# Kernel optimization log

Measured on AMD Instinct MI355X. Metric: run time of the kernel, lower is better.

Reference implementation:

```python
import jax, jax.numpy as jnp
import numpy as np
from math import factorial, sqrt, pi

L = 10  # must match init_kwargs


def setup_inputs() -> dict:
    key = jax.random.key(0)
    pos = jax.random.normal(key, (2_000_000, 3), dtype=jnp.float32)
    return {"pos": pos}


def _cpow_tables(zr, zi, nmax):
    """Powers (zr + i*zi)^n for n=0..nmax. Returns (nmax+1, N) real and imag parts.
    Matches powcmplx in the source (repeated complex multiply), computed once."""
    reals = [jnp.ones_like(zr)]
    imags = [jnp.zeros_like(zr)]
    for _ in range(nmax):
        r, im = reals[-1], imags[-1]
        reals.append(zr * r - zi * im)
        imags.append(zr * im + zi * r)
    return jnp.stack(reals), jnp.stack(imags)


def reference(pos):
    norms = jnp.linalg.norm(pos, axis=1)            # (N,)
    mask = (norms > 0).astype(pos.dtype)            # replaces boolean indexing ids
    x, y, x0 = pos[:, 0], pos[:, 1], pos[:, 2]
    xpl1r, xpl1i = -0.5 * x, -0.5 * y
    xm1r, xm1i = 0.5 * x, -0.5 * y
    # precompute all needed complex powers (same math as powcmplx, deduplicated)
    z1r_t, z1i_t = _cpow_tables(xpl1r, xpl1i, L)    # (L+1, N)
    z2r_t, z2i_t = _cpow_tables(xm1r, xm1i, L)

    clms = [None] * ((L + 1) ** 2)
    i = 0
    for l in range(L + 1):
        rl = norms ** l
        for M in range(-l, 1):
            m = abs(M)
            shr = jnp.zeros_like(x)
            shi = jnp.zeros_like(x)
            for p in range(l + 1):
                q = p - m
                s = l - p - q
                if q >= 0 and s >= 0:
                    z1r, z1i = z1r_t[p], z1i_t[p]
                    z2r, z2i = z2r_t[q], z2i_t[q]
                    # NOTE: faithful to source, including its quirks:
                    # zreal uses z1r**2 - z2i**2, and the term is scaled by x0
                    # (x0**s is computed in the source but never used).
                    zreal = z1r ** 2 - z2i ** 2
                    zimag = z1r * z2i + z1i * z2r
                    c = 1.0 / (factorial(p) * factorial(q) * factorial(s))
                    shr = shr + zreal * x0 * c
                    shi = shi + zimag * x0 * c
            scale = sqrt(factorial(l + m) * factorial(l - m)) * sqrt((2 * l + 1) / (4.0 * pi))
            clm_r = jnp.sum(shr * rl * mask) * scale
            clm_i = jnp.sum(shi * rl * mask) * scale
            if m == 0:
                clms[i] = clm_r
            else:
                f = sqrt(2.0) * (-1) ** m
                clms[i] = f * clm_i
                clms[i + 2 * m] = f * clm_r
            i += 1
        i += l
    return jnp.stack(clms).reshape(-1, 1)  # ((L+1)^2, 1)
```

## Files before the change

### kernel.cpp

```cpp
#include <hip/hip_runtime.h>

namespace {

constexpr int LMAX  = 10;
constexpr int NPART = 2;
constexpr int PART_OF_L[LMAX + 1] = {1, 1, 0, 0, 1, 1, 0, 0, 1, 1, 0};
constexpr double PI_D = 3.14159265358979323846;

constexpr double dfact(int n) {
    double r = 1.0;
    for (int i = 2; i <= n; ++i) r *= (double)i;
    return r;
}

constexpr double csqrt(double x) {
    if (x <= 0.0) return 0.0;
    double g = x > 1.0 ? x : 1.0;
    for (int i = 0; i < 100; ++i) g = 0.5 * (g + x / g);
    return g;
}

constexpr double FACT[LMAX + 1] = {1., 1., 2., 6., 24., 120., 720., 5040., 40320., 362880., 3628800.};

constexpr int slot_base(int part, int l) {
    int c = 0;
    for (int ll = 0; ll < l; ++ll)
        if (PART_OF_L[ll] == part) c += 2 * ll + 1;
    return c;
}
constexpr int nacc_part(int part) {
    int c = 0;
    for (int l = 0; l <= LMAX; ++l)
        if (PART_OF_L[l] == part) c += 2 * l + 1;
    return c;
}
constexpr int part_lmax(int part) {
    int mx = 0;
    for (int l = 0; l <= LMAX; ++l)
        if (PART_OF_L[l] == part) mx = l;
    return mx;
}
constexpr int slot_r(int part, int l, int m) { return slot_base(part, l) + m; }
constexpr int slot_i(int part, int l, int m) { return slot_base(part, l) + (l + 1) + (m - 1); }

constexpr int MAXNA = 61;

constexpr float ci_coef(int l, int m, int q) {
    const double c = 1.0 / (FACT[q + m] * FACT[q] * FACT[l - m - 2 * q]);
    return (q & 1) ? (float)(-c) : (float)c;
}

struct Tables {
    int   map[NPART][MAXNA];
    float scl[NPART][MAXNA];
};

constexpr Tables make_tables() {
    Tables t{};
    for (int part = 0; part < NPART; ++part) {
        for (int l = 0; l <= LMAX; ++l) {
            if (PART_OF_L[l] != part) continue;
            for (int m = 0; m <= l; ++m) {
                const int k = slot_r(part, l, m);
                const double scale =
                    csqrt(dfact(l + m) * dfact(l - m)) * csqrt((2 * l + 1) / (4.0 * PI_D));
                const double fold = (m >= 1 && (l - m) <= 1) ? 1.0 / (dfact(m) * dfact(l - m)) : 1.0;
                if (m == 0) {
                    t.map[part][k] = l * l + l;
                    t.scl[part][k] = (float)(scale * fold);
                } else {
                    const double f = csqrt(2.0) * ((m & 1) ? -1.0 : 1.0);
                    t.map[part][k] = l * l + l + m;
                    t.scl[part][k] = (float)(f * scale * fold);
                }
            }
            for (int m = 1; m <= l; ++m) {
                const int k = slot_i(part, l, m);
                const double scale =
                    csqrt(dfact(l + m) * dfact(l - m)) * csqrt((2 * l + 1) / (4.0 * PI_D));
                const double f    = csqrt(2.0) * ((m & 1) ? -1.0 : 1.0);
                const double fold = ((l - m) <= 1) ? 1.0 / (dfact(m) * dfact(l - m)) : 1.0;
                t.map[part][k] = l * l + l - m;
                t.scl[part][k] = (float)(f * scale * fold);
            }
        }
    }
    return t;
}

__constant__ Tables c_tab = make_tables();

}

template <int PART>
__device__ __forceinline__ void sht_part(const float* __restrict__ pos,
                                         float* __restrict__ out, int n, int nblk) {
    constexpr int NA = nacc_part(PART);
    constexpr int PL = part_lmax(PART);

    float acc[NA];
#pragma unroll
    for (int k = 0; k < NA; ++k) acc[k] = 0.f;

    const int bid    = (int)(blockIdx.x >> 1);
    const int tid    = bid * 256 + (int)threadIdx.x;
    const int stride = nblk * 256;

    int   i = tid;
    float x = 0.f, y = 0.f, z0 = 0.f;
    if (i < n) {
        x  = pos[3 * i + 0];
        y  = pos[3 * i + 1];
        z0 = pos[3 * i + 2];
    }

    while (i < n) {
        const int inext = i + stride;
        float     px = 0.f, py = 0.f, pz = 0.f;
        if (inext < n) {
            px = pos[3 * inext + 0];
            py = pos[3 * inext + 1];
            pz = pos[3 * inext + 2];
        }

        const float r2  = x * x + y * y + z0 * z0;
        const float nrm = sqrtf(r2);
        const float w0  = (nrm > 0.f) ? z0 : 0.f;

        const float ar = -0.5f * x, ai = -0.5f * y;
        const float rho = ar * ar + ai * ai;

        float zi[PL + 1], sr[PL + 1], si[PL + 1];
        zi[0] = 0.f;
        sr[0] = 1.f;
        si[0] = 0.f;
        float zrc = 1.f;
#pragma unroll
        for (int p = 1; p <= PL; ++p) {
            const float nzr = ar * zrc - ai * zi[p - 1];
            zi[p]           = ar * zi[p - 1] + ai * zrc;
            zrc             = nzr;
            sr[p]           = zrc * zrc;
            si[p]           = zi[p] * zi[p];
        }
        float rp[PL + 1];
        rp[0] = 1.f;
#pragma unroll
        for (int l = 1; l <= PL; ++l) rp[l] = rp[l - 1] * nrm;

#pragma unroll
        for (int l = 0; l <= LMAX; ++l) {
            if (PART_OF_L[l] != PART) continue;
            const float wrl = w0 * rp[l];
#pragma unroll
            for (int m = 0; m <= l; ++m) {
                const int Q = (l - m) >> 1;
                if (m >= 1 && Q == 0) {
                    acc[slot_r(PART, l, m)] += sr[m] * wrl;
                    acc[slot_i(PART, l, m)] += zi[m] * wrl;
                } else {
                    float shr = 0.f;
#pragma unroll
                    for (int p = m; 2 * p <= l + m; ++p) {
                        const int   q  = p - m;
                        const float cr = (float)(1.0 / (FACT[p] * FACT[q] * FACT[l - 2 * p + m]));
                        shr += (sr[p] - si[q]) * cr;
                    }
                    acc[slot_r(PART, l, m)] += shr * wrl;
                    if (m >= 1) {
                        float t = ci_coef(l, m, Q);
#pragma unroll
                        for (int q = Q - 1; q >= 0; --q) t = t * rho + ci_coef(l, m, q);
                        acc[slot_i(PART, l, m)] += (t * zi[m]) * wrl;
                    }
                }
            }
        }

        i  = inext;
        x  = px;
        y  = py;
        z0 = pz;
    }

    __shared__ float red[4][NA];
    const int lane = threadIdx.x & 63;
    const int wav  = threadIdx.x >> 6;
#pragma unroll
    for (int k = 0; k < NA; ++k) {
        float v = acc[k];
#pragma unroll
        for (int off = 32; off > 0; off >>= 1) v += __shfl_down(v, off, 64);
        if (lane == 0) red[wav][k] = v;
    }
    __syncthreads();
    if ((int)threadIdx.x < NA) {
        const int   k = (int)threadIdx.x;
        const float v = red[0][k] + red[1][k] + red[2][k] + red[3][k];
        atomicAdd(&out[c_tab.map[PART][k]], v * c_tab.scl[PART][k]);
    }
}

__global__ __launch_bounds__(256, 3) void sht_kernel(const float* __restrict__ pos,
                                                     float* __restrict__ out, int n, int nblk) {
    if (blockIdx.x & 1)
        sht_part<1>(pos, out, n, nblk);
    else
        sht_part<0>(pos, out, n, nblk);
}

extern "C" void kernel_launch(void* const* d_in, const int* in_sizes, int n_in,
                              void* d_out, int out_size, void* d_ws, size_t ws_size,
                              hipStream_t stream) {
    const float* pos = (const float*)d_in[0];
    float* out       = (float*)d_out;
    const int n      = in_sizes[0] / 3;

    hipMemsetAsync(d_out, 0, (size_t)out_size * sizeof(float), stream);

    const int threads       = 256;
    const int nblk_per_part = 384;
    const int blocks        = NPART * nblk_per_part;
    sht_kernel<<<blocks, threads, 0, stream>>>(pos, out, n, nblk_per_part);
}
```

Measured before the change: 123.5 us.

## Process two particles per thread iteration with vectorized float2 loads

Each thread now handles a pair of particles per loop iteration, loading six floats as three float2 values and interleaving the two particles' arithmetic to expose instruction-level parallelism. The si table is shrunk to only the needed entries, and only the radial powers that are actually used are computed. Launch bounds drop from 3 to 2 blocks per CU to make room for the extra registers. The aim is to hide latency through ILP and cut load instructions, at the cost of higher register pressure and lower occupancy, with the same grid size leaving half the threads idle per pair count.

```diff
diff --git a/kernel.cpp b/kernel.cpp
--- a/kernel.cpp
+++ b/kernel.cpp
@@ -39,6 +39,18 @@
     for (int l = 0; l <= LMAX; ++l)
         if (PART_OF_L[l] == part) mx = l;
     return mx;
+}
+constexpr int nls(int part) {
+    int c = 0;
+    for (int l = 0; l <= LMAX; ++l)
+        if (PART_OF_L[l] == part) ++c;
+    return c;
+}
+constexpr int lidx(int part, int l) {
+    int c = 0;
+    for (int ll = 0; ll < l; ++ll)
+        if (PART_OF_L[ll] == part) ++c;
+    return c;
 }
 constexpr int slot_r(int part, int l, int m) { return slot_base(part, l) + m; }
 constexpr int slot_i(int part, int l, int m) { return slot_base(part, l) + (l + 1) + (m - 1); }
@@ -90,6 +102,22 @@
 
 __constant__ Tables c_tab = make_tables();
 
+__device__ __forceinline__ void load_pair(const float* __restrict__ pos, int ip, int n,
+                                          float* __restrict__ c) {
+    const int i0 = 2 * ip;
+    if (i0 + 1 < n) {
+        const float2* p2 = reinterpret_cast<const float2*>(pos + 3 * i0);
+        const float2  a = p2[0], b = p2[1], d = p2[2];
+        c[0] = a.x; c[1] = a.y; c[2] = b.x;
+        c[3] = b.y; c[4] = d.x; c[5] = d.y;
+    } else if (i0 < n) {
+        c[0] = pos[3 * i0]; c[1] = pos[3 * i0 + 1]; c[2] = pos[3 * i0 + 2];
+        c[3] = c[4] = c[5] = 0.f;
+    } else {
+        c[0] = c[1] = c[2] = c[3] = c[4] = c[5] = 0.f;
+    }
+}
+
 }
 
 template <int PART>
@@ -97,6 +125,8 @@
                                          float* __restrict__ out, int n, int nblk) {
     constexpr int NA = nacc_part(PART);
     constexpr int PL = part_lmax(PART);
+    constexpr int QX = PL / 2;
+    constexpr int NL = nls(PART);
 
     float acc[NA];
 #pragma unroll
@@ -105,82 +135,121 @@
     const int bid    = (int)(blockIdx.x >> 1);
     const int tid    = bid * 256 + (int)threadIdx.x;
     const int stride = nblk * 256;
-
-    int   i = tid;
-    float x = 0.f, y = 0.f, z0 = 0.f;
-    if (i < n) {
-        x  = pos[3 * i + 0];
-        y  = pos[3 * i + 1];
-        z0 = pos[3 * i + 2];
-    }
-
-    while (i < n) {
-        const int inext = i + stride;
-        float     px = 0.f, py = 0.f, pz = 0.f;
-        if (inext < n) {
-            px = pos[3 * inext + 0];
-            py = pos[3 * inext + 1];
-            pz = pos[3 * inext + 2];
-        }
-
-        const float r2  = x * x + y * y + z0 * z0;
-        const float nrm = sqrtf(r2);
-        const float w0  = (nrm > 0.f) ? z0 : 0.f;
-
-        const float ar = -0.5f * x, ai = -0.5f * y;
-        const float rho = ar * ar + ai * ai;
-
-        float zi[PL + 1], sr[PL + 1], si[PL + 1];
-        zi[0] = 0.f;
-        sr[0] = 1.f;
-        si[0] = 0.f;
-        float zrc = 1.f;
+    const int npair  = (n + 1) >> 1;
+
+    float cur[6];
+    int   ip = tid;
+    load_pair(pos, ip, n, cur);
+
+    while (ip < npair) {
+        const int inext = ip + stride;
+        float     nxt[6];
+        load_pair(pos, inext, n, nxt);
+
+        const float X[2] = {cur[0], cur[3]};
+        const float Y[2] = {cur[1], cur[4]};
+        const float Z[2] = {cur[2], cur[5]};
+
+        float nrm[2], w0[2], ar[2], ai[2], rho[2];
+#pragma unroll
+        for (int j = 0; j < 2; ++j) {
+            const float r2 = X[j] * X[j] + Y[j] * Y[j] + Z[j] * Z[j];
+            nrm[j] = sqrtf(r2);
+            w0[j]  = (nrm[j] > 0.f) ? Z[j] : 0.f;
+            ar[j]  = -0.5f * X[j];
+            ai[j]  = -0.5f * Y[j];
+            rho[j] = ar[j] * ar[j] + ai[j] * ai[j];
+        }
+
+        float zi[2][PL + 1], sr[2][PL + 1], si[2][QX + 1], zrc[2];
+#pragma unroll
+        for (int j = 0; j < 2; ++j) {
+            zi[j][0] = 0.f;
+            sr[j][0] = 1.f;
+            si[j][0] = 0.f;
+            zrc[j]   = 1.f;
+        }
 #pragma unroll
         for (int p = 1; p <= PL; ++p) {
-            const float nzr = ar * zrc - ai * zi[p - 1];
-            zi[p]           = ar * zi[p - 1] + ai * zrc;
-            zrc             = nzr;
-            sr[p]           = zrc * zrc;
-            si[p]           = zi[p] * zi[p];
-        }
-        float rp[PL + 1];
-        rp[0] = 1.f;
-#pragma unroll
-        for (int l = 1; l <= PL; ++l) rp[l] = rp[l - 1] * nrm;
+#pragma unroll
+            for (int j = 0; j < 2; ++j) {
+                const float nzr = ar[j] * zrc[j] - ai[j] * zi[j][p - 1];
+                zi[j][p]        = ar[j] * zi[j][p - 1] + ai[j] * zrc[j];
+                zrc[j]          = nzr;
+                sr[j][p]        = zrc[j] * zrc[j];
+                if (p <= QX) si[j][p] = zi[j][p] * zi[j][p];
+            }
+        }
+
+        float wl[2][NL];
+#pragma unroll
+        for (int j = 0; j < 2; ++j) {
+            if constexpr (PART == 0) {
+                const float n1 = nrm[j], n2 = n1 * n1, n3 = n2 * n1;
+                const float n6 = n3 * n3, n7 = n6 * n1, n10 = n7 * n3;
+                wl[j][0] = w0[j] * n2;
+                wl[j][1] = w0[j] * n3;
+                wl[j][2] = w0[j] * n6;
+                wl[j][3] = w0[j] * n7;
+                wl[j][4] = w0[j] * n10;
+            } else {
+                const float n1 = nrm[j], n2 = n1 * n1, n4 = n2 * n2;
+                const float n5 = n4 * n1, n8 = n4 * n4, n9 = n8 * n1;
+                wl[j][0] = w0[j];
+                wl[j][1] = w0[j] * n1;
+                wl[j][2] = w0[j] * n4;
+                wl[j][3] = w0[j] * n5;
+                wl[j][4] = w0[j] * n8;
+                wl[j][5] = w0[j] * n9;
+            }
+        }
 
 #pragma unroll
         for (int l = 0; l <= LMAX; ++l) {
             if (PART_OF_L[l] != PART) continue;
-            const float wrl = w0 * rp[l];
+            const int li = lidx(PART, l);
 #pragma unroll
             for (int m = 0; m <= l; ++m) {
                 const int Q = (l - m) >> 1;
                 if (m >= 1 && Q == 0) {
-                    acc[slot_r(PART, l, m)] += sr[m] * wrl;
-                    acc[slot_i(PART, l, m)] += zi[m] * wrl;
+#pragma unroll
+                    for (int j = 0; j < 2; ++j)
+                        acc[slot_r(PART, l, m)] += sr[j][m] * wl[j][li];
+#pragma unroll
+                    for (int j = 0; j < 2; ++j)
+                        acc[slot_i(PART, l, m)] += zi[j][m] * wl[j][li];
                 } else {
-                    float shr = 0.f;
+                    float shr[2] = {0.f, 0.f};
 #pragma unroll
                     for (int p = m; 2 * p <= l + m; ++p) {
                         const int   q  = p - m;
                         const float cr = (float)(1.0 / (FACT[p] * FACT[q] * FACT[l - 2 * p + m]));
-                        shr += (sr[p] - si[q]) * cr;
+#pragma unroll
+                        for (int j = 0; j < 2; ++j) shr[j] += (sr[j][p] - si[j][q]) * cr;
                     }
-                    acc[slot_r(PART, l, m)] += shr * wrl;
+#pragma unroll
+                    for (int j = 0; j < 2; ++j)
+                        acc[slot_r(PART, l, m)] += shr[j] * wl[j][li];
                     if (m >= 1) {
-                        float t = ci_coef(l, m, Q);
-#pragma unroll
-                        for (int q = Q - 1; q >= 0; --q) t = t * rho + ci_coef(l, m, q);
-                        acc[slot_i(PART, l, m)] += (t * zi[m]) * wrl;
+                        float t[2];
+                        t[0] = t[1] = ci_coef(l, m, Q);
+#pragma unroll
+                        for (int q = Q - 1; q >= 0; --q) {
+                            const float c = ci_coef(l, m, q);
+#pragma unroll
+                            for (int j = 0; j < 2; ++j) t[j] = t[j] * rho[j] + c;
+                        }
+#pragma unroll
+                        for (int j = 0; j < 2; ++j)
+                            acc[slot_i(PART, l, m)] += (t[j] * zi[j][m]) * wl[j][li];
                     }
                 }
             }
         }
 
-        i  = inext;
-        x  = px;
-        y  = py;
-        z0 = pz;
+        ip = inext;
+#pragma unroll
+        for (int k = 0; k < 6; ++k) cur[k] = nxt[k];
     }
 
     __shared__ float red[4][NA];
@@ -201,7 +270,7 @@
     }
 }
 
-__global__ __launch_bounds__(256, 3) void sht_kernel(const float* __restrict__ pos,
+__global__ __launch_bounds__(256, 2) void sht_kernel(const float* __restrict__ pos,
                                                      float* __restrict__ out, int n, int nblk) {
     if (blockIdx.x & 1)
         sht_part<1>(pos, out, n, nblk);
@@ -218,7 +287,7 @@
 
     hipMemsetAsync(d_out, 0, (size_t)out_size * sizeof(float), stream);
 
-    const int threads       = 256;
+    const int threads = 256;
     const int nblk_per_part = 384;
     const int blocks        = NPART * nblk_per_part;
     sht_kernel<<<blocks, threads, 0, stream>>>(pos, out, n, nblk_per_part);
```

New measurement: 120.2 us. 2.7% less time.
